# Kernel optimization log

Hardware: AMD Instinct MI355X
Metric: run time of the kernel (lower is better)

## Reference

```python
import jax, jax.numpy as jnp
import numpy as np

D = 512      # feature_dim
DK = 64      # key_feature_dim
LQ = 2048
LK = 2048
B = 16
EPS = 1e-9


def _l2norm(x, axis=-1, eps=1e-12):
    # matches torch F.normalize(p=2): x / max(||x||, eps)
    n = jnp.sqrt(jnp.sum(x * x, axis=axis, keepdims=True))
    return x / jnp.maximum(n, eps)


def setup_inputs() -> dict:
    key = jax.random.key(0)
    ks = jax.random.split(key, 7)
    std = np.sqrt(2.0 / DK)
    stdv = np.sqrt(2.0 / D)
    return {
        "query": jax.random.normal(ks[0], (LQ, B, D), jnp.float32),
        "key": jax.random.normal(ks[1], (LK, B, D), jnp.float32),
        "value": jax.random.normal(ks[2], (LK, B, D), jnp.float32),
        "WK": jax.random.normal(ks[3], (DK, D), jnp.float32) * std,
        "WQ": jax.random.normal(ks[4], (DK, D), jnp.float32) * std,
        "WV": jax.random.normal(ks[5], (D, D), jnp.float32) * stdv,
        "Wt": jax.random.normal(ks[6], (D, D), jnp.float32) * (1.0 / np.sqrt(D)),  # trans_conv weight
    }


def reference(query, key, value, WK, WQ, WV, Wt):
    # q/k projections + cosine normalization; tensors are [L, B, *]
    w_k = _l2norm(key @ WK.T)      # [LK, B, DK]
    w_q = _l2norm(query @ WQ.T)    # [LQ, B, DK]
    # dot_prod: [B, LQ, LK]
    dot = jnp.einsum('qbd,kbd->bqk', w_q, w_k)
    affinity = jax.nn.softmax(dot, axis=-1)  # temp = 1
    # second renorm over the query axis (dim=1)
    affinity = affinity / (EPS + jnp.sum(affinity, axis=1, keepdims=True))
    w_v = value @ WV.T                        # [LK, B, D]
    out = jnp.einsum('bqk,kbd->qbd', affinity, w_v)  # [LQ, B, D]
    out = (query - out) @ Wt.T
    return jax.nn.relu(out)
```

## Files before the change

### kernel.cpp

```cpp
#include <hip/hip_runtime.h>

#define LQ 2048
#define LK 2048
#define BB 16
#define DD 512
#define DKK 64
#define EPSF 1e-9f

typedef unsigned short u16;
typedef unsigned char u8;
typedef long i64;
typedef __attribute__((ext_vector_type(8))) short bf16x8;
typedef __attribute__((ext_vector_type(4))) float f32x4;
#define MFMA16(a, b, c) __builtin_amdgcn_mfma_f32_16x16x32_bf16(a, b, c, 0, 0, 0)
#define MFMAF8(a, b, c) __builtin_amdgcn_mfma_f32_16x16x32_fp8_fp8(a, b, c, 0, 0, 0)

__device__ inline u16 f2bf(float f) {
    unsigned int u = __float_as_uint(f);
    u += 0x7fffu + ((u >> 16) & 1u);
    return (u16)(u >> 16);
}
__device__ inline bf16x8 cvt8(float4 a, float4 b) {
    bf16x8 r;
    r[0] = (short)f2bf(a.x); r[1] = (short)f2bf(a.y); r[2] = (short)f2bf(a.z); r[3] = (short)f2bf(a.w);
    r[4] = (short)f2bf(b.x); r[5] = (short)f2bf(b.y); r[6] = (short)f2bf(b.z); r[7] = (short)f2bf(b.w);
    return r;
}
__device__ inline int pk_fp8x4(float a, float b, float c, float d) {
    int r = __builtin_amdgcn_cvt_pk_fp8_f32(a, b, 0, false);
    r = __builtin_amdgcn_cvt_pk_fp8_f32(c, d, r, true);
    return r;
}
__device__ inline void gload16(const void* g, void* l) {
    __builtin_amdgcn_global_load_lds((const __attribute__((address_space(1))) unsigned int*)g,
                                     (__attribute__((address_space(3))) unsigned int*)l, 16, 0, 0);
}

__global__ __launch_bounds__(256) void k_cvt(const float* __restrict__ src, u16* __restrict__ dst, int n) {
    int i = (blockIdx.x * 256 + threadIdx.x) * 4;
    if (i < n) {
        float4 v = *reinterpret_cast<const float4*>(src + i);
        *reinterpret_cast<ushort4*>(dst + i) = make_ushort4(f2bf(v.x), f2bf(v.y), f2bf(v.z), f2bf(v.w));
    }
}

__global__ __launch_bounds__(256) void k_cvtv(const float* __restrict__ value, u16* __restrict__ vb) {
    size_t i = ((size_t)blockIdx.x * 256 + threadIdx.x) * 8;
    int k = (int)(i >> 13);
    int r = (int)(i & 8191);
    int b = r >> 9, d = r & 511;
    float4 a = *reinterpret_cast<const float4*>(value + i);
    float4 c = *reinterpret_cast<const float4*>(value + i + 4);
    *reinterpret_cast<bf16x8*>(vb + ((size_t)b * LK + k) * DD + d) = cvt8(a, c);
}

__global__ __launch_bounds__(256) void k_projqk(const float* __restrict__ xq, const float* __restrict__ xk,
                                                const u16* __restrict__ Wq, const u16* __restrict__ Wk,
                                                u16* __restrict__ yq, u16* __restrict__ yk)
{
    const float* x = blockIdx.z ? xk : xq;
    const u16* Wb = blockIdx.z ? Wk : Wq;
    u16* y = blockIdx.z ? yk : yq;
    const int b = blockIdx.y, r0 = blockIdx.x * 64;
    const int tid = threadIdx.x, wave = tid >> 6, lane = tid & 63, l15 = lane & 15, g = lane >> 4;
    const int rw = r0 + wave * 16;
    f32x4 z = {0.f, 0.f, 0.f, 0.f};
    f32x4 acc[4];
#pragma unroll
    for (int nf = 0; nf < 4; nf++) acc[nf] = z;

    for (int kt = 0; kt < DD; kt += 32) {
        const float* p = x + ((size_t)(rw + l15) * BB + b) * DD + kt + g * 8;
        bf16x8 af = cvt8(*reinterpret_cast<const float4*>(p), *reinterpret_cast<const float4*>(p + 4));
#pragma unroll
        for (int nf = 0; nf < 4; nf++) {
            bf16x8 bf_ = *reinterpret_cast<const bf16x8*>(Wb + (size_t)(nf * 16 + l15) * DD + kt + g * 8);
            acc[nf] = MFMA16(af, bf_, acc[nf]);
        }
    }
    float rn[4];
#pragma unroll
    for (int j = 0; j < 4; j++) {
        float t2 = acc[0][j] * acc[0][j] + acc[1][j] * acc[1][j]
                 + acc[2][j] * acc[2][j] + acc[3][j] * acc[3][j];
        t2 += __shfl_xor(t2, 1, 64);
        t2 += __shfl_xor(t2, 2, 64);
        t2 += __shfl_xor(t2, 4, 64);
        t2 += __shfl_xor(t2, 8, 64);
        rn[j] = 1.f / fmaxf(sqrtf(t2), 1e-12f);
    }
#pragma unroll
    for (int nf = 0; nf < 4; nf++)
#pragma unroll
        for (int j = 0; j < 4; j++) {
            int q = rw + g * 4 + j;
            y[((size_t)b * LQ + q) * DKK + nf * 16 + l15] = f2bf(acc[nf][j] * rn[j]);
        }
}

__global__ __launch_bounds__(256) void k_score(const u16* __restrict__ wqb, const u16* __restrict__ wkb,
                                               u8* __restrict__ E0t, float* __restrict__ Rpart, int b0)
{
    const int bx = blockIdx.x, qc = blockIdx.y, bl = blockIdx.z, b = b0 + bl;
    const int tid = threadIdx.x, w = tid >> 6, lane = tid & 63, l15 = lane & 15, g = lane >> 4;
    const int kt0 = bx * 8 + w * 2;
    f32x4 z = {0.f, 0.f, 0.f, 0.f};

    bf16x8 af[2][2];
#pragma unroll
    for (int j = 0; j < 2; j++) {
        const u16* ar = wkb + ((size_t)b * LK + (kt0 + j) * 16 + l15) * DKK;
        af[j][0] = *reinterpret_cast<const bf16x8*>(ar + g * 8);
        af[j][1] = *reinterpret_cast<const bf16x8*>(ar + 32 + g * 8);
    }
    u8* Eb = E0t + (size_t)bl * LQ * LK + l15 * 16 + g * 4;
    float* Rp0 = Rpart + ((size_t)bl * 128 + kt0) * LQ + qc * 512;
    float* Rp1 = Rp0 + LQ;
    const u16* qbase = wqb + ((size_t)b * LQ + qc * 512 + l15) * DKK + g * 8;

    bf16x8 c0 = *reinterpret_cast<const bf16x8*>(qbase);
    bf16x8 c1 = *reinterpret_cast<const bf16x8*>(qbase + 32);
    bf16x8 n0_ = c0, n1_ = c1;

#pragma unroll 4
    for (int qf = 0; qf < 32; qf++) {
        if (qf < 31) {
            const u16* br = qbase + (size_t)(qf + 1) * 16 * DKK;
            n0_ = *reinterpret_cast<const bf16x8*>(br);
            n1_ = *reinterpret_cast<const bf16x8*>(br + 32);
        }
        __builtin_amdgcn_sched_barrier(0);
        int qt = qc * 32 + qf;
#pragma unroll
        for (int j = 0; j < 2; j++) {
            f32x4 s = z;
            s = MFMA16(af[j][0], c0, s);
            s = MFMA16(af[j][1], c1, s);
            float pe0 = __expf(s[0]), pe1 = __expf(s[1]);
            float pe2 = __expf(s[2]), pe3 = __expf(s[3]);
            *reinterpret_cast<int*>(Eb + ((size_t)qt * 128 + kt0 + j) * 256) =
                pk_fp8x4(pe0, pe1, pe2, pe3);
            float v = pe0 + pe1 + pe2 + pe3;
            v += __shfl_xor(v, 16, 64);
            v += __shfl_xor(v, 32, 64);
            if (g == 0) (j ? Rp1 : Rp0)[qf * 16 + l15] = v;
        }
        c0 = n0_; c1 = n1_;
    }
}

__global__ __launch_bounds__(256) void k_rsum(const float* __restrict__ Rpart, float* __restrict__ Rq, int b0) {
    int idx = blockIdx.x * 256 + threadIdx.x;
    int bl = idx >> 11, q = idx & 2047;
    const float* rp = Rpart + (size_t)bl * 128 * LQ + q;
    float s = 0.f;
    for (int p = 0; p < 128; p++) s += rp[(size_t)p * LQ];
    Rq[(size_t)(b0 + bl) * LQ + q] = 1.f / s;
}

__global__ __launch_bounds__(256) void k_colsum(const u8* __restrict__ E0t, const float* __restrict__ Rq,
                                                float* __restrict__ Cpart, int b0)
{
    const int qc = blockIdx.y, bl = blockIdx.z;
    const int tid = threadIdx.x, w = tid >> 6, lane = tid & 63, l15 = lane & 15, g = lane >> 4;
    const int kt = blockIdx.x * 4 + w;
    const u8* base = E0t + (size_t)bl * LQ * LK + (size_t)kt * 256 + l15 * 16 + g * 4;
    const float* rq = Rq + (size_t)(b0 + bl) * LQ;
    float acc[4] = {0.f, 0.f, 0.f, 0.f};
#pragma unroll 4
    for (int i = 0; i < 32; i++) {
        int qt = qc * 32 + i;
        unsigned int u = *reinterpret_cast<const unsigned int*>(base + (size_t)qt * 32768);
        float wgt = rq[qt * 16 + l15];
#pragma unroll
        for (int by = 0; by < 4; by++) {
            unsigned int f = 0x3C000000u + (((u >> (8 * by)) & 0x7Fu) << 20);
            acc[by] += __uint_as_float(f) * wgt;
        }
    }
#pragma unroll
    for (int by = 0; by < 4; by++) {
        acc[by] += __shfl_xor(acc[by], 1, 64);
        acc[by] += __shfl_xor(acc[by], 2, 64);
        acc[by] += __shfl_xor(acc[by], 4, 64);
        acc[by] += __shfl_xor(acc[by], 8, 64);
    }
    if (l15 == 0) {
        float4 v4 = make_float4(acc[0], acc[1], acc[2], acc[3]);
        *reinterpret_cast<float4*>(Cpart + ((size_t)bl * 4 + qc) * LK + kt * 16 + g * 4) = v4;
    }
}

__global__ __launch_bounds__(256) void k_csum(const float* __restrict__ Cpart, float* __restrict__ ci, int b0) {
    int idx = blockIdx.x * 256 + threadIdx.x;
    int bl = idx >> 11, k = idx & 2047;
    const float* cp = Cpart + (size_t)bl * 4 * LK + k;
    float s = 0.f;
#pragma unroll
    for (int p = 0; p < 4; p++) s += cp[(size_t)p * LK];
    ci[(size_t)(b0 + bl) * LK + k] = 1.f / (EPSF + s);
}

__global__ __launch_bounds__(256, 3) void k_projv(const u16* __restrict__ vb, const u16* __restrict__ WVb,
                                                  const float* __restrict__ ci, u8* __restrict__ wvS, int b0)
{
    const int b = b0 + blockIdx.z, k0 = blockIdx.x * 128, n0 = blockIdx.y * 128;
    const int tid = threadIdx.x, wv = tid >> 6, lane = tid & 63, l15 = lane & 15, g = lane >> 4;
    const int qg = wv >> 1, dg = wv & 1;

    __shared__ __align__(16) u16 As[128 * 64], Bs[128 * 64];

    const int srow = wv * 8 + (lane >> 3);
    const int scb = ((lane & 7) * 16) ^ ((srow & 7) << 4);
    const char* gA = (const char*)(vb + ((size_t)b * LK + k0 + srow) * DD) + scb;
    const char* gB = (const char*)(WVb + (size_t)(n0 + srow) * DD) + scb;
    const size_t rstep = (size_t)32 * DD * 2;

    f32x4 z = {0.f, 0.f, 0.f, 0.f};
    f32x4 acc[4][4];
#pragma unroll
    for (int m = 0; m < 4; m++)
#pragma unroll
        for (int nf = 0; nf < 4; nf++) acc[m][nf] = z;

#pragma unroll
    for (int p = 0; p < 4; ++p) {
        gload16(gA + p * rstep, (char*)As + p * 4096 + wv * 1024);
        gload16(gB + p * rstep, (char*)Bs + p * 4096 + wv * 1024);
    }

    for (int tt = 0; tt < DD / 64; ++tt) {
        __syncthreads();
        bf16x8 af[4][2], bv[4][2];
#pragma unroll
        for (int m = 0; m < 4; m++) {
            int row = qg * 64 + m * 16 + l15;
            const char* rp = (const char*)As + row * 128;
            int x = (row & 7) << 4;
#pragma unroll
            for (int kk = 0; kk < 2; kk++)
                af[m][kk] = *reinterpret_cast<const bf16x8*>(rp + ((kk * 64 + g * 16) ^ x));
        }
#pragma unroll
        for (int nf = 0; nf < 4; nf++) {
            int row = dg * 64 + nf * 16 + l15;
            const char* rp = (const char*)Bs + row * 128;
            int x = (row & 7) << 4;
#pragma unroll
            for (int kk = 0; kk < 2; kk++)
                bv[nf][kk] = *reinterpret_cast<const bf16x8*>(rp + ((kk * 64 + g * 16) ^ x));
        }
        __syncthreads();
        if (tt + 1 < DD / 64) {
            int ktb = (tt + 1) * 128;
#pragma unroll
            for (int p = 0; p < 4; ++p) {
                gload16(gA + p * rstep + ktb, (char*)As + p * 4096 + wv * 1024);
                gload16(gB + p * rstep + ktb, (char*)Bs + p * 4096 + wv * 1024);
            }
        }
#pragma unroll
        for (int nf = 0; nf < 4; nf++)
#pragma unroll
            for (int m = 0; m < 4; m++) {
                acc[m][nf] = MFMA16(af[m][0], bv[nf][0], acc[m][nf]);
                acc[m][nf] = MFMA16(af[m][1], bv[nf][1], acc[m][nf]);
            }
    }
#pragma unroll
    for (int m = 0; m < 4; m++) {
        float cv[4];
        int kb = k0 + qg * 64 + m * 16 + g * 4;
#pragma unroll
        for (int j = 0; j < 4; j++) cv[j] = ci[(size_t)b * LK + kb + j];
#pragma unroll
        for (int nf = 0; nf < 4; nf++) {
            int d = n0 + dg * 64 + nf * 16 + l15;
            *reinterpret_cast<int*>(wvS + ((size_t)b * DD + d) * LK + kb) =
                pk_fp8x4(acc[m][nf][0] * cv[0], acc[m][nf][1] * cv[1],
                         acc[m][nf][2] * cv[2], acc[m][nf][3] * cv[3]);
        }
    }
}

__global__ __launch_bounds__(256, 3) void k_pvgemm(const float* __restrict__ query,
                                                   const u8* __restrict__ E0t,
                                                   const u8* __restrict__ wvS,
                                                   const float* __restrict__ Rq,
                                                   u16* __restrict__ tout, int b0, int G)
{
    const int i = blockIdx.x;
    int bl, tile;
    if (G == 16) { bl = (i & 7) + 8 * (i >> 9); tile = (i >> 3) & 63; }
    else         { bl = i % G; tile = i / G; }
    const int b = b0 + bl;
    const int q0 = (tile >> 2) * 128, n0 = (tile & 3) * 128;
    const int tid = threadIdx.x, wv = tid >> 6, lane = tid & 63, l15 = lane & 15, g = lane >> 4;
    const int qg = wv >> 1, dg = wv & 1;

    __shared__ __align__(16) char As[16384], Bs[16384];

    const u8* Eb = E0t + (size_t)bl * LQ * LK;
    const u8* Vb = wvS + (size_t)b * DD * LK;

    const char* gAt = (const char*)Eb + (size_t)(q0 >> 4) * 128 * 256;
    const int srow = wv * 8 + (lane >> 3);
    const int scb = ((lane & 7) * 16) ^ ((srow & 7) << 4);
    const char* gB = (const char*)Vb + (size_t)(n0 + srow) * LK + scb;
    const size_t rstepB = (size_t)32 * LK;

    f32x4 z = {0.f, 0.f, 0.f, 0.f};
    f32x4 acc[4][4];
#pragma unroll
    for (int m = 0; m < 4; m++)
#pragma unroll
        for (int nf = 0; nf < 4; nf++) acc[m][nf] = z;

    auto stage = [&](int t) {
#pragma unroll
        for (int p = 0; p < 4; ++p) {
            int c = wv * 4 + p;
            gload16(gAt + ((size_t)(c >> 1) * 128 + t * 8) * 256 + (c & 1) * 1024 + lane * 16,
                    (char*)As + c * 1024);
            gload16(gB + p * rstepB + t * 128, (char*)Bs + p * 4096 + wv * 1024);
        }
    };
    stage(0);

    for (int t = 0; t < LK / 128; ++t) {
        __syncthreads();
        i64 af[4][4], bv[4][4];
#pragma unroll
        for (int m = 0; m < 4; m++) {
            const char* rp = (const char*)As + (qg * 4 + m) * 2048 + l15 * 16 + (g & 1) * 8;
#pragma unroll
            for (int kk = 0; kk < 4; kk++)
                af[m][kk] = *reinterpret_cast<const i64*>(rp + (kk * 2 + (g >> 1)) * 256);
        }
#pragma unroll
        for (int nf = 0; nf < 4; nf++) {
            int row = dg * 64 + nf * 16 + l15;
            const char* rp = (const char*)Bs + row * 128;
            int x = (row & 7) << 4;
#pragma unroll
            for (int kk = 0; kk < 4; kk++)
                bv[nf][kk] = *reinterpret_cast<const i64*>(rp + ((kk * 32 + g * 8) ^ x));
        }
        __syncthreads();
        if (t + 1 < LK / 128) stage(t + 1);
#pragma unroll
        for (int kk = 0; kk < 4; kk++)
#pragma unroll
            for (int nf = 0; nf < 4; nf++)
#pragma unroll
                for (int m = 0; m < 4; m++)
                    acc[m][nf] = MFMAF8(af[m][kk], bv[nf][kk], acc[m][nf]);
    }
#pragma unroll
    for (int m = 0; m < 4; m++) {
        float rqv[4];
#pragma unroll
        for (int j = 0; j < 4; j++)
            rqv[j] = Rq[(size_t)b * LQ + q0 + qg * 64 + m * 16 + g * 4 + j];
#pragma unroll
        for (int nf = 0; nf < 4; nf++)
#pragma unroll
            for (int j = 0; j < 4; j++) {
                int q = q0 + qg * 64 + m * 16 + g * 4 + j;
                int d = n0 + dg * 64 + nf * 16 + l15;
                size_t idx = ((size_t)q * BB + b) * DD + d;
                tout[idx] = f2bf(query[idx] - acc[m][nf][j] * rqv[j]);
            }
    }
}

__global__ __launch_bounds__(256, 3) void k_final(const u16* __restrict__ t, const u16* __restrict__ Wtb,
                                                  float* __restrict__ out)
{
    const int r0 = blockIdx.x * 128, n0 = blockIdx.y * 128;
    const int tid = threadIdx.x, wv = tid >> 6, lane = tid & 63, l15 = lane & 15, g = lane >> 4;
    const int qg = wv >> 1, dg = wv & 1;

    __shared__ __align__(16) u16 As[128 * 64], Bs[128 * 64];

    const int srow = wv * 8 + (lane >> 3);
    const int scb = ((lane & 7) * 16) ^ ((srow & 7) << 4);
    const char* gA = (const char*)(t + (size_t)(r0 + srow) * DD) + scb;
    const char* gB = (const char*)(Wtb + (size_t)(n0 + srow) * DD) + scb;
    const size_t rstep = (size_t)32 * DD * 2;

    f32x4 z = {0.f, 0.f, 0.f, 0.f};
    f32x4 acc[4][4];
#pragma unroll
    for (int m = 0; m < 4; m++)
#pragma unroll
        for (int nf = 0; nf < 4; nf++) acc[m][nf] = z;

#pragma unroll
    for (int p = 0; p < 4; ++p) {
        gload16(gA + p * rstep, (char*)As + p * 4096 + wv * 1024);
        gload16(gB + p * rstep, (char*)Bs + p * 4096 + wv * 1024);
    }

    for (int tt = 0; tt < DD / 64; ++tt) {
        __syncthreads();
        bf16x8 af[4][2], bv[4][2];
#pragma unroll
        for (int m = 0; m < 4; m++) {
            int row = qg * 64 + m * 16 + l15;
            const char* rp = (const char*)As + row * 128;
            int x = (row & 7) << 4;
#pragma unroll
            for (int kk = 0; kk < 2; kk++)
                af[m][kk] = *reinterpret_cast<const bf16x8*>(rp + ((kk * 64 + g * 16) ^ x));
        }
#pragma unroll
        for (int nf = 0; nf < 4; nf++) {
            int row = dg * 64 + nf * 16 + l15;
            const char* rp = (const char*)Bs + row * 128;
            int x = (row & 7) << 4;
#pragma unroll
            for (int kk = 0; kk < 2; kk++)
                bv[nf][kk] = *reinterpret_cast<const bf16x8*>(rp + ((kk * 64 + g * 16) ^ x));
        }
        __syncthreads();
        if (tt + 1 < DD / 64) {
            int ktb = (tt + 1) * 128;
#pragma unroll
            for (int p = 0; p < 4; ++p) {
                gload16(gA + p * rstep + ktb, (char*)As + p * 4096 + wv * 1024);
                gload16(gB + p * rstep + ktb, (char*)Bs + p * 4096 + wv * 1024);
            }
        }
#pragma unroll
        for (int nf = 0; nf < 4; nf++)
#pragma unroll
            for (int m = 0; m < 4; m++) {
                acc[m][nf] = MFMA16(af[m][0], bv[nf][0], acc[m][nf]);
                acc[m][nf] = MFMA16(af[m][1], bv[nf][1], acc[m][nf]);
            }
    }
#pragma unroll
    for (int m = 0; m < 4; m++)
#pragma unroll
        for (int nf = 0; nf < 4; nf++)
#pragma unroll
            for (int j = 0; j < 4; j++)
                out[(size_t)(r0 + qg * 64 + m * 16 + g * 4 + j) * DD + n0 + dg * 64 + nf * 16 + l15] =
                    fmaxf(acc[m][nf][j], 0.f);
}

extern "C" void kernel_launch(void* const* d_in, const int* in_sizes, int n_in,
                              void* d_out, int out_size, void* d_ws, size_t ws_size,
                              hipStream_t stream)
{
    const float* query = (const float*)d_in[0];
    const float* key   = (const float*)d_in[1];
    const float* value = (const float*)d_in[2];
    const float* WK    = (const float*)d_in[3];
    const float* WQ    = (const float*)d_in[4];
    const float* WV    = (const float*)d_in[5];
    const float* Wt    = (const float*)d_in[6];
    float* out = (float*)d_out;

    char* ws = (char*)d_ws;
    u16*   wqb = (u16*)(ws);
    u16*   wkb = (u16*)(ws + (4u << 20));
    u8*    wvS = (u8*)(ws + (8u << 20));
    u16*   t   = (u16*)(ws + (24u << 20));
    u16*   vb  = (u16*)(ws + (56u << 20));
    float* Rq  = (float*)(ws + (88u << 20));
    float* ci  = (float*)(ws + (88u << 20) + (128u << 10));
    u16*   WQb = (u16*)(ws + (88u << 20) + (256u << 10));
    u16*   WKb = (u16*)(ws + (88u << 20) + (320u << 10));
    u16*   WVb = (u16*)(ws + (88u << 20) + (384u << 10));
    u16*   Wtb = (u16*)(ws + (88u << 20) + (896u << 10));

    const size_t fixed = 90ull << 20;
    const size_t perG = (4ull << 20) + (1ull << 20) + (32ull << 10);
    int G = 0;
    for (int g = 16; g >= 1; g >>= 1)
        if (fixed + (size_t)g * perG <= ws_size) { G = g; break; }
    if (G == 0) G = 1;
    u8*    E0    = (u8*)(ws + fixed);
    float* Rpart = (float*)(ws + fixed + ((size_t)G << 22));
    float* Cpart = (float*)(ws + fixed + ((size_t)G << 22) + ((size_t)G << 20));

    k_cvt<<<32, 256, 0, stream>>>(WQ, WQb, DKK * DD);
    k_cvt<<<32, 256, 0, stream>>>(WK, WKb, DKK * DD);
    k_cvt<<<256, 256, 0, stream>>>(WV, WVb, DD * DD);
    k_cvt<<<256, 256, 0, stream>>>(Wt, Wtb, DD * DD);
    k_cvtv<<<8192, 256, 0, stream>>>(value, vb);

    k_projqk<<<dim3(LQ / 64, BB, 2), 256, 0, stream>>>(query, key, WQb, WKb, wqb, wkb);

    for (int b0 = 0; b0 < BB; b0 += G) {
        k_score<<<dim3(LK / 128, LQ / 512, G), 256, 0, stream>>>(wqb, wkb, E0, Rpart, b0);
        k_rsum<<<G * 8, 256, 0, stream>>>(Rpart, Rq, b0);
        k_colsum<<<dim3(32, 4, G), 256, 0, stream>>>(E0, Rq, Cpart, b0);
        k_csum<<<G * 8, 256, 0, stream>>>(Cpart, ci, b0);
        k_projv<<<dim3(LK / 128, DD / 128, G), 256, 0, stream>>>(vb, WVb, ci, wvS, b0);
        k_pvgemm<<<64 * G, 256, 0, stream>>>(query, E0, wvS, Rq, t, b0, G);
    }

    k_final<<<dim3(LQ * BB / 128, DD / 128), 256, 0, stream>>>(t, Wtb, out);
}
```

Baseline: 276.0 us.

## Fuse value fp32-to-bf16 conversion into projv and LDS-pipeline projqk

Removes the separate k_cvtv pass that converted and transposed value into a bf16 buffer. k_projv now stages fp32 value rows into double-buffered LDS and converts to bf16 while building MFMA fragments, reading WV straight from global memory. k_projqk likewise moves to 128-row tiles with double-buffered LDS staging of fp32 inputs instead of per-lane global loads. The aim is to cut a full read/write round trip of the value tensor and improve load coalescing. The cost is that projv reads value four times (once per n-tile) in fp32, twice the bytes of bf16, and the WV fragments bypass LDS.

```diff
diff --git a/kernel.cpp b/kernel.cpp
--- a/kernel.cpp
+++ b/kernel.cpp
@@ -44,16 +44,6 @@
     }
 }
 
-__global__ __launch_bounds__(256) void k_cvtv(const float* __restrict__ value, u16* __restrict__ vb) {
-    size_t i = ((size_t)blockIdx.x * 256 + threadIdx.x) * 8;
-    int k = (int)(i >> 13);
-    int r = (int)(i & 8191);
-    int b = r >> 9, d = r & 511;
-    float4 a = *reinterpret_cast<const float4*>(value + i);
-    float4 c = *reinterpret_cast<const float4*>(value + i + 4);
-    *reinterpret_cast<bf16x8*>(vb + ((size_t)b * LK + k) * DD + d) = cvt8(a, c);
-}
-
 __global__ __launch_bounds__(256) void k_projqk(const float* __restrict__ xq, const float* __restrict__ xk,
                                                 const u16* __restrict__ Wq, const u16* __restrict__ Wk,
                                                 u16* __restrict__ yq, u16* __restrict__ yk)
@@ -61,41 +51,72 @@
     const float* x = blockIdx.z ? xk : xq;
     const u16* Wb = blockIdx.z ? Wk : Wq;
     u16* y = blockIdx.z ? yk : yq;
-    const int b = blockIdx.y, r0 = blockIdx.x * 64;
-    const int tid = threadIdx.x, wave = tid >> 6, lane = tid & 63, l15 = lane & 15, g = lane >> 4;
-    const int rw = r0 + wave * 16;
+    const int b = blockIdx.y, r0 = blockIdx.x * 128;
+    const int tid = threadIdx.x, wv = tid >> 6, lane = tid & 63, l15 = lane & 15, g = lane >> 4;
+
+    __shared__ __align__(16) float As[2][128 * 32];
+
+    const int srow = wv * 8 + (lane >> 3);
+    const int scb = ((lane & 7) * 16) ^ ((srow & 7) << 4);
+
     f32x4 z = {0.f, 0.f, 0.f, 0.f};
-    f32x4 acc[4];
-#pragma unroll
-    for (int nf = 0; nf < 4; nf++) acc[nf] = z;
-
-    for (int kt = 0; kt < DD; kt += 32) {
-        const float* p = x + ((size_t)(rw + l15) * BB + b) * DD + kt + g * 8;
-        bf16x8 af = cvt8(*reinterpret_cast<const float4*>(p), *reinterpret_cast<const float4*>(p + 4));
+    f32x4 acc[2][4];
+#pragma unroll
+    for (int m = 0; m < 2; m++)
+#pragma unroll
+        for (int nf = 0; nf < 4; nf++) acc[m][nf] = z;
+
+    auto stage = [&](int buf, int kt) {
+#pragma unroll
+        for (int p = 0; p < 4; ++p) {
+            const char* src = (const char*)(x + ((size_t)(r0 + p * 32 + srow) * BB + b) * DD) + kt * 4 + scb;
+            gload16(src, (char*)As[buf] + p * 4096 + wv * 1024);
+        }
+    };
+    stage(0, 0);
+    int buf = 0;
+    for (int tt = 0; tt < 16; ++tt) {
+        __syncthreads();
+        if (tt + 1 < 16) stage(buf ^ 1, (tt + 1) * 32);
+        bf16x8 af[2];
+#pragma unroll
+        for (int m = 0; m < 2; m++) {
+            int row = wv * 32 + m * 16 + l15;
+            const char* rp = (const char*)As[buf] + row * 128;
+            int xs = (row & 7) << 4;
+            float4 fa = *reinterpret_cast<const float4*>(rp + ((g * 32) ^ xs));
+            float4 fb = *reinterpret_cast<const float4*>(rp + ((g * 32 + 16) ^ xs));
+            af[m] = cvt8(fa, fb);
+        }
 #pragma unroll
         for (int nf = 0; nf < 4; nf++) {
-            bf16x8 bf_ = *reinterpret_cast<const bf16x8*>(Wb + (size_t)(nf * 16 + l15) * DD + kt + g * 8);
-            acc[nf] = MFMA16(af, bf_, acc[nf]);
-        }
-    }
-    float rn[4];
-#pragma unroll
-    for (int j = 0; j < 4; j++) {
-        float t2 = acc[0][j] * acc[0][j] + acc[1][j] * acc[1][j]
-                 + acc[2][j] * acc[2][j] + acc[3][j] * acc[3][j];
-        t2 += __shfl_xor(t2, 1, 64);
-        t2 += __shfl_xor(t2, 2, 64);
-        t2 += __shfl_xor(t2, 4, 64);
-        t2 += __shfl_xor(t2, 8, 64);
-        rn[j] = 1.f / fmaxf(sqrtf(t2), 1e-12f);
-    }
-#pragma unroll
-    for (int nf = 0; nf < 4; nf++)
+            bf16x8 bw = *reinterpret_cast<const bf16x8*>(Wb + (size_t)(nf * 16 + l15) * DD + tt * 32 + g * 8);
+            acc[0][nf] = MFMA16(af[0], bw, acc[0][nf]);
+            acc[1][nf] = MFMA16(af[1], bw, acc[1][nf]);
+        }
+        buf ^= 1;
+    }
+#pragma unroll
+    for (int m = 0; m < 2; m++) {
+        float rn[4];
 #pragma unroll
         for (int j = 0; j < 4; j++) {
-            int q = rw + g * 4 + j;
-            y[((size_t)b * LQ + q) * DKK + nf * 16 + l15] = f2bf(acc[nf][j] * rn[j]);
-        }
+            float t2 = acc[m][0][j] * acc[m][0][j] + acc[m][1][j] * acc[m][1][j]
+                     + acc[m][2][j] * acc[m][2][j] + acc[m][3][j] * acc[m][3][j];
+            t2 += __shfl_xor(t2, 1, 64);
+            t2 += __shfl_xor(t2, 2, 64);
+            t2 += __shfl_xor(t2, 4, 64);
+            t2 += __shfl_xor(t2, 8, 64);
+            rn[j] = 1.f / fmaxf(sqrtf(t2), 1e-12f);
+        }
+#pragma unroll
+        for (int nf = 0; nf < 4; nf++)
+#pragma unroll
+            for (int j = 0; j < 4; j++) {
+                int q = r0 + wv * 32 + m * 16 + g * 4 + j;
+                y[((size_t)b * LQ + q) * DKK + nf * 16 + l15] = f2bf(acc[m][nf][j] * rn[j]);
+            }
+    }
 }
 
 __global__ __launch_bounds__(256) void k_score(const u16* __restrict__ wqb, const u16* __restrict__ wkb,
@@ -201,20 +222,17 @@
     ci[(size_t)(b0 + bl) * LK + k] = 1.f / (EPSF + s);
 }
 
-__global__ __launch_bounds__(256, 3) void k_projv(const u16* __restrict__ vb, const u16* __restrict__ WVb,
-                                                  const float* __restrict__ ci, u8* __restrict__ wvS, int b0)
+__global__ __launch_bounds__(256) void k_projv(const float* __restrict__ value, const u16* __restrict__ WVb,
+                                               const float* __restrict__ ci, u8* __restrict__ wvS, int b0)
 {
     const int b = b0 + blockIdx.z, k0 = blockIdx.x * 128, n0 = blockIdx.y * 128;
     const int tid = threadIdx.x, wv = tid >> 6, lane = tid & 63, l15 = lane & 15, g = lane >> 4;
     const int qg = wv >> 1, dg = wv & 1;
 
-    __shared__ __align__(16) u16 As[128 * 64], Bs[128 * 64];
+    __shared__ __align__(16) float As[2][128 * 32];
 
     const int srow = wv * 8 + (lane >> 3);
     const int scb = ((lane & 7) * 16) ^ ((srow & 7) << 4);
-    const char* gA = (const char*)(vb + ((size_t)b * LK + k0 + srow) * DD) + scb;
-    const char* gB = (const char*)(WVb + (size_t)(n0 + srow) * DD) + scb;
-    const size_t rstep = (size_t)32 * DD * 2;
 
     f32x4 z = {0.f, 0.f, 0.f, 0.f};
     f32x4 acc[4][4];
@@ -223,49 +241,35 @@
 #pragma unroll
         for (int nf = 0; nf < 4; nf++) acc[m][nf] = z;
 
-#pragma unroll
-    for (int p = 0; p < 4; ++p) {
-        gload16(gA + p * rstep, (char*)As + p * 4096 + wv * 1024);
-        gload16(gB + p * rstep, (char*)Bs + p * 4096 + wv * 1024);
-    }
-
-    for (int tt = 0; tt < DD / 64; ++tt) {
+    auto stage = [&](int buf, int kt) {
+#pragma unroll
+        for (int p = 0; p < 4; ++p) {
+            const char* src = (const char*)(value + ((size_t)(k0 + p * 32 + srow) * BB + b) * DD) + kt * 4 + scb;
+            gload16(src, (char*)As[buf] + p * 4096 + wv * 1024);
+        }
+    };
+    stage(0, 0);
+    int buf = 0;
+    for (int tt = 0; tt < 16; ++tt) {
         __syncthreads();
-        bf16x8 af[4][2], bv[4][2];
+        if (tt + 1 < 16) stage(buf ^ 1, (tt + 1) * 32);
+        bf16x8 af[4];
 #pragma unroll
         for (int m = 0; m < 4; m++) {
             int row = qg * 64 + m * 16 + l15;
-            const char* rp = (const char*)As + row * 128;
-            int x = (row & 7) << 4;
-#pragma unroll
-            for (int kk = 0; kk < 2; kk++)
-                af[m][kk] = *reinterpret_cast<const bf16x8*>(rp + ((kk * 64 + g * 16) ^ x));
+            const char* rp = (const char*)As[buf] + row * 128;
+            int xs = (row & 7) << 4;
+            float4 fa = *reinterpret_cast<const float4*>(rp + ((g * 32) ^ xs));
+            float4 fb = *reinterpret_cast<const float4*>(rp + ((g * 32 + 16) ^ xs));
+            af[m] = cvt8(fa, fb);
         }
 #pragma unroll
         for (int nf = 0; nf < 4; nf++) {
-            int row = dg * 64 + nf * 16 + l15;
-            const char* rp = (const char*)Bs + row * 128;
-            int x = (row & 7) << 4;
-#pragma unroll
-            for (int kk = 0; kk < 2; kk++)
-                bv[nf][kk] = *reinterpret_cast<const bf16x8*>(rp + ((kk * 64 + g * 16) ^ x));
-        }
-        __syncthreads();
-        if (tt + 1 < DD / 64) {
-            int ktb = (tt + 1) * 128;
-#pragma unroll
-            for (int p = 0; p < 4; ++p) {
-                gload16(gA + p * rstep + ktb, (char*)As + p * 4096 + wv * 1024);
-                gload16(gB + p * rstep + ktb, (char*)Bs + p * 4096 + wv * 1024);
-            }
-        }
-#pragma unroll
-        for (int nf = 0; nf < 4; nf++)
-#pragma unroll
-            for (int m = 0; m < 4; m++) {
-                acc[m][nf] = MFMA16(af[m][0], bv[nf][0], acc[m][nf]);
-                acc[m][nf] = MFMA16(af[m][1], bv[nf][1], acc[m][nf]);
-            }
+            bf16x8 bw = *reinterpret_cast<const bf16x8*>(WVb + (size_t)(n0 + dg * 64 + nf * 16 + l15) * DD + tt * 32 + g * 8);
+#pragma unroll
+            for (int m = 0; m < 4; m++) acc[m][nf] = MFMA16(af[m], bw, acc[m][nf]);
+        }
+        buf ^= 1;
     }
 #pragma unroll
     for (int m = 0; m < 4; m++) {
@@ -468,7 +472,6 @@
     u16*   wkb = (u16*)(ws + (4u << 20));
     u8*    wvS = (u8*)(ws + (8u << 20));
     u16*   t   = (u16*)(ws + (24u << 20));
-    u16*   vb  = (u16*)(ws + (56u << 20));
     float* Rq  = (float*)(ws + (88u << 20));
     float* ci  = (float*)(ws + (88u << 20) + (128u << 10));
     u16*   WQb = (u16*)(ws + (88u << 20) + (256u << 10));
@@ -490,16 +493,15 @@
     k_cvt<<<32, 256, 0, stream>>>(WK, WKb, DKK * DD);
     k_cvt<<<256, 256, 0, stream>>>(WV, WVb, DD * DD);
     k_cvt<<<256, 256, 0, stream>>>(Wt, Wtb, DD * DD);
-    k_cvtv<<<8192, 256, 0, stream>>>(value, vb);
-
-    k_projqk<<<dim3(LQ / 64, BB, 2), 256, 0, stream>>>(query, key, WQb, WKb, wqb, wkb);
+
+    k_projqk<<<dim3(LQ / 128, BB, 2), 256, 0, stream>>>(query, key, WQb, WKb, wqb, wkb);
 
     for (int b0 = 0; b0 < BB; b0 += G) {
         k_score<<<dim3(LK / 128, LQ / 512, G), 256, 0, stream>>>(wqb, wkb, E0, Rpart, b0);
         k_rsum<<<G * 8, 256, 0, stream>>>(Rpart, Rq, b0);
         k_colsum<<<dim3(32, 4, G), 256, 0, stream>>>(E0, Rq, Cpart, b0);
         k_csum<<<G * 8, 256, 0, stream>>>(Cpart, ci, b0);
-        k_projv<<<dim3(LK / 128, DD / 128, G), 256, 0, stream>>>(vb, WVb, ci, wvS, b0);
+        k_projv<<<dim3(LK / 128, DD / 128, G), 256, 0, stream>>>(value, WVb, ci, wvS, b0);
         k_pvgemm<<<64 * G, 256, 0, stream>>>(query, E0, wvS, Rq, t, b0, G);
     }
 
```

New measurement: 257.9 us. 1.07x faster.
